# Performance work log

Measured on AMD Instinct MI355X. Metric: run time of the kernel, lower is better.

Reference implementation:

```python
import jax, jax.numpy as jnp
import numpy as np

D_MODEL = 1024
N_HEADS = 16


def setup_inputs() -> dict:
    key = jax.random.key(0)
    ks = jax.random.split(key, 16)
    B, L, S, D = 4, 2048, 2048, D_MODEL
    inp = {
        "q": jax.random.normal(ks[0], (B, L, D), jnp.float32),
        "k": jax.random.normal(ks[1], (B, S, D), jnp.float32),
        "v": jax.random.normal(ks[2], (B, S, D), jnp.float32),
        "tau": jax.random.uniform(ks[3], (B, 1), jnp.float32, 0.5, 1.5),
        "delta": jax.random.normal(ks[4], (B, S), jnp.float32),
    }
    s = 1.0 / np.sqrt(D)
    inp["Wq"] = jax.random.normal(ks[5], (D, D), jnp.float32) * s
    inp["bq"] = jnp.zeros((D,), jnp.float32)
    inp["Wk"] = jax.random.normal(ks[6], (D, D), jnp.float32) * s
    inp["bk"] = jnp.zeros((D,), jnp.float32)
    inp["Wv"] = jax.random.normal(ks[7], (D, D), jnp.float32) * s
    inp["bv"] = jnp.zeros((D,), jnp.float32)
    inp["Wo"] = jax.random.normal(ks[8], (D, D), jnp.float32) * s
    inp["bo"] = jnp.zeros((D,), jnp.float32)
    return inp


def reference(q, k, v, tau, delta, Wq, bq, Wk, bk, Wv, bv, Wo, bo):
    B, L, D = q.shape
    S = k.shape[1]
    H = N_HEADS
    E = D // H
    # Linear projections (torch Linear: x @ W.T + b), split heads
    qh = (q @ Wq.T + bq).reshape(B, L, H, E)
    kh = (k @ Wk.T + bk).reshape(B, S, H, E)
    vh = (v @ Wv.T + bv).reshape(B, S, H, E)
    scale = 1.0 / np.sqrt(E).astype(np.float32)
    # de-stationary attention: scores * tau + delta, then scaled softmax
    scores = jnp.einsum('blhe,bshe->bhls', qh, kh)
    scores = scores * tau[:, None, None, :] + delta[:, None, None, :]
    a = jax.nn.softmax(scale * scores, axis=-1)  # dropout: eval mode (identity)
    out = jnp.einsum('bhls,bshd->blhd', a, vh).reshape(B, L, D)
    return out @ Wo.T + bo
```

## Files before the change

kernel.cpp:

```cpp
#include <hip/hip_runtime.h>
#include <hip/hip_bf16.h>
#include <stdint.h>

typedef unsigned short u16;
typedef __attribute__((ext_vector_type(8))) short short8;
typedef __attribute__((ext_vector_type(4))) short short4v;
typedef __attribute__((ext_vector_type(4))) float f32x4;
typedef __attribute__((ext_vector_type(2))) unsigned int uint2v;

#define DEV static __device__ __forceinline__

DEV u16 f2bf(float f) {
  union { float f; unsigned u; } x; x.f = f;
  unsigned r = x.u + 0x7FFFu + ((x.u >> 16) & 1u);
  return (u16)(r >> 16);
}

DEV unsigned cvtpk_bf16(float a, float b) {
  unsigned r;
  asm("v_cvt_pk_bf16_f32 %0, %1, %2" : "=v"(r) : "v"(a), "v"(b));
  return r;
}

DEV void gld_lds16(const void* g, void* l) {
  __builtin_amdgcn_global_load_lds(
      (const __attribute__((address_space(1))) unsigned int*)(g),
      (__attribute__((address_space(3))) unsigned int*)(l),
      16, 0, 0);
}

__global__ void cvt3(const float* __restrict__ a, const float* __restrict__ b,
                     const float* __restrict__ c, u16* __restrict__ oa,
                     u16* __restrict__ ob, u16* __restrict__ oc, int n4) {
  int i = blockIdx.x * blockDim.x + threadIdx.x;
  if (i >= n4) return;
  const float* in = (blockIdx.y == 0) ? a : (blockIdx.y == 1) ? b : c;
  u16* out = (blockIdx.y == 0) ? oa : (blockIdx.y == 1) ? ob : oc;
  float4 v = ((const float4*)in)[i];
  short4v o;
  o[0] = (short)f2bf(v.x); o[1] = (short)f2bf(v.y);
  o[2] = (short)f2bf(v.z); o[3] = (short)f2bf(v.w);
  ((short4v*)out)[i] = o;
}

__global__ void cvt4(const float* __restrict__ a, const float* __restrict__ b,
                     const float* __restrict__ c, const float* __restrict__ d,
                     u16* __restrict__ oa, u16* __restrict__ ob,
                     u16* __restrict__ oc, u16* __restrict__ od, int n4) {
  int i = blockIdx.x * blockDim.x + threadIdx.x;
  if (i >= n4) return;
  const float* in = (blockIdx.y == 0) ? a : (blockIdx.y == 1) ? b : (blockIdx.y == 2) ? c : d;
  u16* out = (blockIdx.y == 0) ? oa : (blockIdx.y == 1) ? ob : (blockIdx.y == 2) ? oc : od;
  float4 v = ((const float4*)in)[i];
  short4v o;
  o[0] = (short)f2bf(v.x); o[1] = (short)f2bf(v.y);
  o[2] = (short)f2bf(v.z); o[3] = (short)f2bf(v.w);
  ((short4v*)out)[i] = o;
}

__global__ void scale_delta(const float* __restrict__ in, float* __restrict__ out, int n4) {
  int i = blockIdx.x * blockDim.x + threadIdx.x;
  if (i >= n4) return;
  constexpr float C = 0.125f * 1.44269504f;
  float4 v = ((const float4*)in)[i];
  f32x4 o = {v.x * C, v.y * C, v.z * C, v.w * C};
  ((f32x4*)out)[i] = o;
}

template<int OMODE>
__global__ __launch_bounds__(256, 2)
void gemm_nt(const u16* __restrict__ A, const u16* __restrict__ Bt,
             const float* __restrict__ bias, void* __restrict__ out) {
  constexpr int Mn = 8192, Nn = 1024, Kn = 1024;
  constexpr int BM = 128, BN = 128, BK = 64;
  __shared__ __align__(16) u16 As[BM * BK];
  __shared__ __align__(16) u16 Bs[BN * BK];
  constexpr int nbn = Nn / BN;
  constexpr int nwg = (Mn / BM) * nbn;
  int bid = blockIdx.x;
  int swz = (bid & 7) * (nwg >> 3) + (bid >> 3);
  int bm = (swz / nbn) * BM;
  int bn = (swz % nbn) * BN;
  int tid = threadIdx.x;
  int lane = tid & 63, w = tid >> 6;
  int l15 = lane & 15, l4 = lane >> 4;
  int wm = (w >> 1) * 64, wn = (w & 1) * 64;
  int swl = (w << 6);

  f32x4 acc[4][4];
#pragma unroll
  for (int i = 0; i < 4; ++i)
#pragma unroll
    for (int j = 0; j < 4; ++j) acc[i][j] = (f32x4){0.f, 0.f, 0.f, 0.f};

  const u16* Ag = A + (size_t)bm * Kn;
  const u16* Bg = Bt + (size_t)bn * Kn;

  for (int kt = 0; kt < Kn / BK; ++kt) {
    int k0 = kt * BK;
#pragma unroll
    for (int j = 0; j < 4; ++j) {
      int flat = j * 256 + tid;
      int row = flat >> 3, u = flat & 7;
      int gu = u ^ (row & 7);
      gld_lds16(Ag + (size_t)row * Kn + k0 + gu * 8, &As[(j * 256 + swl) * 8]);
    }
#pragma unroll
    for (int j = 0; j < 4; ++j) {
      int flat = j * 256 + tid;
      int row = flat >> 3, u = flat & 7;
      int gu = u ^ (row & 7);
      gld_lds16(Bg + (size_t)row * Kn + k0 + gu * 8, &Bs[(j * 256 + swl) * 8]);
    }
    __syncthreads();
#pragma unroll
    for (int ks = 0; ks < 2; ++ks) {
      short8 af[4], bfr[4];
#pragma unroll
      for (int i = 0; i < 4; ++i) {
        int ra = wm + i * 16 + l15;
        int ua = (ks * 4 + l4) ^ (ra & 7);
        af[i] = *(const short8*)&As[ra * 64 + ua * 8];
        int rb = wn + i * 16 + l15;
        int ub = (ks * 4 + l4) ^ (rb & 7);
        bfr[i] = *(const short8*)&Bs[rb * 64 + ub * 8];
      }
#pragma unroll
      for (int mi = 0; mi < 4; ++mi)
#pragma unroll
        for (int ni = 0; ni < 4; ++ni)
          acc[mi][ni] = __builtin_amdgcn_mfma_f32_16x16x32_bf16(af[mi], bfr[ni], acc[mi][ni], 0, 0, 0);
    }
    __syncthreads();
  }

#pragma unroll
  for (int ni = 0; ni < 4; ++ni) {
    int n = bn + wn + ni * 16 + l15;
    float bv = bias[n];
    int h = n >> 6, e = n & 63;
#pragma unroll
    for (int mi = 0; mi < 4; ++mi) {
      int m0 = bm + wm + mi * 16 + l4 * 4;
      if (OMODE == 2) {
        float* o = (float*)out;
#pragma unroll
        for (int j = 0; j < 4; ++j)
          o[(size_t)(m0 + j) * Nn + n] = acc[mi][ni][j] + bv;
      } else if (OMODE == 0) {
        u16* o = (u16*)out;
#pragma unroll
        for (int j = 0; j < 4; ++j) {
          int m = m0 + j;
          int b = m >> 11, l = m & 2047;
          int idx = ((b * 16 + h) * 2048 + l) * 64 + e;
          o[idx] = f2bf(acc[mi][ni][j] + bv);
        }
      } else {
        u16* o = (u16*)out;
        int b = m0 >> 11, s = m0 & 2047;
        short4v pk;
#pragma unroll
        for (int j = 0; j < 4; ++j) pk[j] = (short)f2bf(acc[mi][ni][j] + bv);
        int idx = ((b * 16 + h) * 64 + e) * 2048 + s;
        *(short4v*)&o[idx] = pk;
      }
    }
  }
}

__global__ __launch_bounds__(512, 6)
void flash_attn(const u16* __restrict__ qh, const u16* __restrict__ kh,
                const u16* __restrict__ vt, const float* __restrict__ tau,
                const float* __restrict__ dl2g, u16* __restrict__ attn) {
  constexpr int S = 2048, E = 64;
  __shared__ __align__(16) u16 Ks[2][64 * 64];
  __shared__ __align__(16) u16 Vs[2][64 * 64];
  __shared__ __align__(16) float dls[2][64];
  __shared__ __align__(16) u16 Ps[8][16 * 72];

  int bh = blockIdx.x & 63, qb = blockIdx.x >> 6;
  int b = bh >> 4, h = bh & 15;
  int tid = threadIdx.x, lane = tid & 63, w = tid >> 6;
  int l15 = lane & 15, l4 = lane >> 4;
  int q0 = qb * 128 + w * 16;

  int srow = tid >> 3, su = tid & 7, sgu = su ^ (srow & 7);
  u16* ldsKbase0 = &Ks[0][(size_t)(w * 64) * 8];
  u16* ldsKbase1 = &Ks[1][(size_t)(w * 64) * 8];
  u16* ldsVbase0 = &Vs[0][(size_t)(w * 64) * 8];
  u16* ldsVbase1 = &Vs[1][(size_t)(w * 64) * 8];

  const u16* Qg = qh + ((size_t)bh * S + q0) * E;
  short8 qf[2];
  qf[0] = *(const short8*)&Qg[l15 * E + l4 * 8];
  qf[1] = *(const short8*)&Qg[l15 * E + 32 + l4 * 8];

  float st2 = tau[b] * (0.125f * 1.44269504f);
  float l_run = 0.f;
  f32x4 oacc[4];
#pragma unroll
  for (int i = 0; i < 4; ++i) oacc[i] = (f32x4){0.f, 0.f, 0.f, 0.f};

  const u16* Kg = kh + (size_t)bh * S * E;
  const u16* Vg = vt + (size_t)bh * E * S;
  const float* Dg = dl2g + (size_t)b * S;

  gld_lds16(Kg + (size_t)srow * E + sgu * 8, ldsKbase0);
  gld_lds16(Vg + (size_t)srow * S + sgu * 8, ldsVbase0);
  if (tid < 16) gld_lds16(Dg + tid * 4, &dls[0][0]);
  __syncthreads();

  for (int t = 0; t < S / 64; ++t) {
    int cur = t & 1;
    if (t < S / 64 - 1) {
      int s1 = (t + 1) * 64;
      gld_lds16(Kg + (size_t)(s1 + srow) * E + sgu * 8, cur ? ldsKbase0 : ldsKbase1);
      gld_lds16(Vg + (size_t)srow * S + s1 + sgu * 8, cur ? ldsVbase0 : ldsVbase1);
      if (tid < 16) gld_lds16(Dg + s1 + tid * 4, &dls[cur ^ 1][0]);
    }

    f32x4 sc[4];
#pragma unroll
    for (int i = 0; i < 4; ++i) sc[i] = (f32x4){0.f, 0.f, 0.f, 0.f};
    __builtin_amdgcn_s_setprio(1);
#pragma unroll
    for (int ks = 0; ks < 2; ++ks) {
#pragma unroll
      for (int sg = 0; sg < 4; ++sg) {
        int sr = sg * 16 + l15;
        int u = (ks * 4 + l4) ^ (sr & 7);
        short8 kf = *(const short8*)&Ks[cur][sr * 64 + u * 8];
        sc[sg] = __builtin_amdgcn_mfma_f32_16x16x32_bf16(kf, qf[ks], sc[sg], 0, 0, 0);
      }
    }
    __builtin_amdgcn_s_setprio(0);

    float psum = 0.f;
#pragma unroll
    for (int sg = 0; sg < 4; ++sg) {
      f32x4 dlv = *(const f32x4*)&dls[cur][sg * 16 + l4 * 4];
      float p0 = __builtin_amdgcn_exp2f(sc[sg][0] * st2 + dlv[0]);
      float p1 = __builtin_amdgcn_exp2f(sc[sg][1] * st2 + dlv[1]);
      float p2 = __builtin_amdgcn_exp2f(sc[sg][2] * st2 + dlv[2]);
      float p3 = __builtin_amdgcn_exp2f(sc[sg][3] * st2 + dlv[3]);
      psum += (p0 + p1) + (p2 + p3);
      uint2v pk;
      pk[0] = cvtpk_bf16(p0, p1);
      pk[1] = cvtpk_bf16(p2, p3);
      *(uint2v*)&Ps[w][l15 * 72 + sg * 16 + l4 * 4] = pk;
    }
    psum += __shfl_xor(psum, 16);
    psum += __shfl_xor(psum, 32);
    l_run += psum;

    __builtin_amdgcn_s_setprio(1);
#pragma unroll
    for (int ks = 0; ks < 2; ++ks) {
      short8 pf = *(const short8*)&Ps[w][l15 * 72 + ks * 32 + l4 * 8];
#pragma unroll
      for (int ni = 0; ni < 4; ++ni) {
        int er = ni * 16 + l15;
        int u = (ks * 4 + l4) ^ (er & 7);
        short8 vf = *(const short8*)&Vs[cur][er * 64 + u * 8];
        oacc[ni] = __builtin_amdgcn_mfma_f32_16x16x32_bf16(pf, vf, oacc[ni], 0, 0, 0);
      }
    }
    __builtin_amdgcn_s_setprio(0);
    __syncthreads();
  }

  float li[4];
#pragma unroll
  for (int j = 0; j < 4; ++j) li[j] = 1.f / __shfl(l_run, l4 * 4 + j);
#pragma unroll
  for (int ni = 0; ni < 4; ++ni) {
    int e = ni * 16 + l15;
#pragma unroll
    for (int j = 0; j < 4; ++j) {
      int l = q0 + l4 * 4 + j;
      size_t idx = (((size_t)b * 2048 + l) * 16 + h) * 64 + e;
      attn[idx] = f2bf(oacc[ni][j] * li[j]);
    }
  }
}

extern "C" void kernel_launch(void* const* d_in, const int* in_sizes, int n_in,
                              void* d_out, int out_size, void* d_ws, size_t ws_size,
                              hipStream_t stream) {
  const float* q = (const float*)d_in[0];
  const float* k = (const float*)d_in[1];
  const float* v = (const float*)d_in[2];
  const float* tau = (const float*)d_in[3];
  const float* delta = (const float*)d_in[4];
  const float* Wq = (const float*)d_in[5];
  const float* bq = (const float*)d_in[6];
  const float* Wk = (const float*)d_in[7];
  const float* bk = (const float*)d_in[8];
  const float* Wv = (const float*)d_in[9];
  const float* bv = (const float*)d_in[10];
  const float* Wo = (const float*)d_in[11];
  const float* bo = (const float*)d_in[12];

  const size_t SZ_ACT = (size_t)8192 * 1024 * 2;
  const size_t SZ_W = (size_t)1024 * 1024 * 2;
  char* p = (char*)d_ws;
  u16* qbf = (u16*)p; p += SZ_ACT;
  u16* kbf = (u16*)p; p += SZ_ACT;
  u16* vbf = (u16*)p; p += SZ_ACT;
  u16* wq = (u16*)p; p += SZ_W;
  u16* wk = (u16*)p; p += SZ_W;
  u16* wv = (u16*)p; p += SZ_W;
  u16* wo = (u16*)p; p += SZ_W;
  float* dl2g = (float*)p; p += 8192 * 4;
  u16* qhb = (u16*)p; p += SZ_ACT;
  u16* khb = (u16*)p; p += SZ_ACT;
  u16* vtb = (u16*)p; p += SZ_ACT;
  u16* attn = qbf;

  cvt3<<<dim3(8192, 3), 256, 0, stream>>>(q, k, v, qbf, kbf, vbf, 2097152);
  cvt4<<<dim3(1024, 4), 256, 0, stream>>>(Wq, Wk, Wv, Wo, wq, wk, wv, wo, 262144);
  scale_delta<<<8, 256, 0, stream>>>(delta, dl2g, 2048);

  gemm_nt<0><<<512, 256, 0, stream>>>(qbf, wq, bq, qhb);
  gemm_nt<0><<<512, 256, 0, stream>>>(kbf, wk, bk, khb);
  gemm_nt<1><<<512, 256, 0, stream>>>(vbf, wv, bv, vtb);
  flash_attn<<<1024, 512, 0, stream>>>(qhb, khb, vtb, tau, dl2g, attn);
  gemm_nt<2><<<512, 256, 0, stream>>>(attn, wo, bo, d_out);
}
```

Measured before the change: 222.5 us.

## Switch flash attention to 32x32x16 MFMA with register-resident P via permlane swap

Rewrites the attention inner loop to use 32x32x16 bf16 MFMAs, with each wave handling 32 query rows instead of 16, which halves the grid to 512 blocks. The probability tile stays in registers: it is repacked with v_permlane32_swap instead of going through an LDS round trip, which removes the per-wave Ps buffer and its LDS traffic. Each K/V tile loaded into LDS now feeds twice as many query rows, and the output store is vectorized. In exchange, register pressure rises, so launch bounds drop to 4 waves per SIMD, and the smaller grid lowers occupancy and parallelism.

```diff
diff --git a/kernel.cpp b/kernel.cpp
--- a/kernel.cpp
+++ b/kernel.cpp
@@ -6,7 +6,9 @@
 typedef __attribute__((ext_vector_type(8))) short short8;
 typedef __attribute__((ext_vector_type(4))) short short4v;
 typedef __attribute__((ext_vector_type(4))) float f32x4;
+typedef __attribute__((ext_vector_type(16))) float f32x16;
 typedef __attribute__((ext_vector_type(2))) unsigned int uint2v;
+typedef __attribute__((ext_vector_type(4))) unsigned int uint4v;
 
 #define DEV static __device__ __forceinline__
 
@@ -20,6 +22,10 @@
   unsigned r;
   asm("v_cvt_pk_bf16_f32 %0, %1, %2" : "=v"(r) : "v"(a), "v"(b));
   return r;
+}
+
+DEV void pl32swap(unsigned& a, unsigned& b) {
+  asm("v_permlane32_swap_b32 %0, %1" : "+v"(a), "+v"(b));
 }
 
 DEV void gld_lds16(const void* g, void* l) {
@@ -27,6 +33,11 @@
       (const __attribute__((address_space(1))) unsigned int*)(g),
       (__attribute__((address_space(3))) unsigned int*)(l),
       16, 0, 0);
+}
+
+DEV f32x16 zero16() {
+  f32x16 z = {0.f,0.f,0.f,0.f,0.f,0.f,0.f,0.f,0.f,0.f,0.f,0.f,0.f,0.f,0.f,0.f};
+  return z;
 }
 
 __global__ void cvt3(const float* __restrict__ a, const float* __restrict__ b,
@@ -169,7 +180,33 @@
   }
 }
 
-__global__ __launch_bounds__(512, 6)
+DEV float softpack(const f32x16 sc, float st2, const float* dlp, int hi,
+                   short8& f0, short8& f1) {
+  float pe[16];
+#pragma unroll
+  for (int g = 0; g < 4; ++g) {
+    f32x4 dlv = *(const f32x4*)(dlp + g * 8 + hi * 4);
+#pragma unroll
+    for (int m = 0; m < 4; ++m)
+      pe[g * 4 + m] = __builtin_amdgcn_exp2f(sc[g * 4 + m] * st2 + dlv[m]);
+  }
+  float ps = 0.f;
+#pragma unroll
+  for (int i = 0; i < 16; i += 4) ps += (pe[i] + pe[i + 1]) + (pe[i + 2] + pe[i + 3]);
+  unsigned a0 = cvtpk_bf16(pe[0], pe[1]), a1 = cvtpk_bf16(pe[2], pe[3]);
+  unsigned b0 = cvtpk_bf16(pe[4], pe[5]), b1 = cvtpk_bf16(pe[6], pe[7]);
+  pl32swap(a0, b0);
+  pl32swap(a1, b1);
+  f0 = __builtin_bit_cast(short8, (uint4v){a0, a1, b0, b1});
+  unsigned c0 = cvtpk_bf16(pe[8], pe[9]), c1 = cvtpk_bf16(pe[10], pe[11]);
+  unsigned d0 = cvtpk_bf16(pe[12], pe[13]), d1 = cvtpk_bf16(pe[14], pe[15]);
+  pl32swap(c0, d0);
+  pl32swap(c1, d1);
+  f1 = __builtin_bit_cast(short8, (uint4v){c0, c1, d0, d1});
+  return ps;
+}
+
+__global__ __launch_bounds__(512, 4)
 void flash_attn(const u16* __restrict__ qh, const u16* __restrict__ kh,
                 const u16* __restrict__ vt, const float* __restrict__ tau,
                 const float* __restrict__ dl2g, u16* __restrict__ attn) {
@@ -177,111 +214,88 @@
   __shared__ __align__(16) u16 Ks[2][64 * 64];
   __shared__ __align__(16) u16 Vs[2][64 * 64];
   __shared__ __align__(16) float dls[2][64];
-  __shared__ __align__(16) u16 Ps[8][16 * 72];
 
   int bh = blockIdx.x & 63, qb = blockIdx.x >> 6;
   int b = bh >> 4, h = bh & 15;
   int tid = threadIdx.x, lane = tid & 63, w = tid >> 6;
-  int l15 = lane & 15, l4 = lane >> 4;
-  int q0 = qb * 128 + w * 16;
-
-  int srow = tid >> 3, su = tid & 7, sgu = su ^ (srow & 7);
-  u16* ldsKbase0 = &Ks[0][(size_t)(w * 64) * 8];
-  u16* ldsKbase1 = &Ks[1][(size_t)(w * 64) * 8];
-  u16* ldsVbase0 = &Vs[0][(size_t)(w * 64) * 8];
-  u16* ldsVbase1 = &Vs[1][(size_t)(w * 64) * 8];
+  int l31 = lane & 31, hi = lane >> 5;
+  int q0 = qb * 256 + w * 32;
+
+  int srow = tid >> 3, sgu = (tid & 7) ^ ((tid >> 3) & 7);
 
   const u16* Qg = qh + ((size_t)bh * S + q0) * E;
-  short8 qf[2];
-  qf[0] = *(const short8*)&Qg[l15 * E + l4 * 8];
-  qf[1] = *(const short8*)&Qg[l15 * E + 32 + l4 * 8];
+  short8 qf[4];
+#pragma unroll
+  for (int ec = 0; ec < 4; ++ec)
+    qf[ec] = *(const short8*)&Qg[l31 * E + ec * 16 + hi * 8];
 
   float st2 = tau[b] * (0.125f * 1.44269504f);
   float l_run = 0.f;
-  f32x4 oacc[4];
-#pragma unroll
-  for (int i = 0; i < 4; ++i) oacc[i] = (f32x4){0.f, 0.f, 0.f, 0.f};
+  f32x16 oa0 = zero16(), oa1 = zero16();
 
   const u16* Kg = kh + (size_t)bh * S * E;
   const u16* Vg = vt + (size_t)bh * E * S;
   const float* Dg = dl2g + (size_t)b * S;
 
-  gld_lds16(Kg + (size_t)srow * E + sgu * 8, ldsKbase0);
-  gld_lds16(Vg + (size_t)srow * S + sgu * 8, ldsVbase0);
+  gld_lds16(Kg + (size_t)srow * E + sgu * 8, &Ks[0][w * 512]);
+  gld_lds16(Vg + (size_t)srow * S + sgu * 8, &Vs[0][w * 512]);
   if (tid < 16) gld_lds16(Dg + tid * 4, &dls[0][0]);
   __syncthreads();
 
   for (int t = 0; t < S / 64; ++t) {
-    int cur = t & 1;
+    int cur = t & 1, nxt = cur ^ 1;
     if (t < S / 64 - 1) {
       int s1 = (t + 1) * 64;
-      gld_lds16(Kg + (size_t)(s1 + srow) * E + sgu * 8, cur ? ldsKbase0 : ldsKbase1);
-      gld_lds16(Vg + (size_t)srow * S + s1 + sgu * 8, cur ? ldsVbase0 : ldsVbase1);
-      if (tid < 16) gld_lds16(Dg + s1 + tid * 4, &dls[cur ^ 1][0]);
-    }
-
-    f32x4 sc[4];
-#pragma unroll
-    for (int i = 0; i < 4; ++i) sc[i] = (f32x4){0.f, 0.f, 0.f, 0.f};
+      gld_lds16(Kg + (size_t)(s1 + srow) * E + sgu * 8, &Ks[nxt][w * 512]);
+      gld_lds16(Vg + (size_t)srow * S + s1 + sgu * 8, &Vs[nxt][w * 512]);
+      if (tid < 16) gld_lds16(Dg + s1 + tid * 4, &dls[nxt][0]);
+    }
+
+    const char* KsB = (const char*)&Ks[cur][0];
+    f32x16 sc0 = zero16(), sc1 = zero16();
     __builtin_amdgcn_s_setprio(1);
 #pragma unroll
-    for (int ks = 0; ks < 2; ++ks) {
-#pragma unroll
-      for (int sg = 0; sg < 4; ++sg) {
-        int sr = sg * 16 + l15;
-        int u = (ks * 4 + l4) ^ (sr & 7);
-        short8 kf = *(const short8*)&Ks[cur][sr * 64 + u * 8];
-        sc[sg] = __builtin_amdgcn_mfma_f32_16x16x32_bf16(kf, qf[ks], sc[sg], 0, 0, 0);
-      }
+    for (int ec = 0; ec < 4; ++ec) {
+      int uo = (((ec * 2 + hi) ^ (l31 & 7)) * 16) + l31 * 128;
+      short8 kf0 = *(const short8*)(KsB + uo);
+      short8 kf1 = *(const short8*)(KsB + 4096 + uo);
+      sc0 = __builtin_amdgcn_mfma_f32_32x32x16_bf16(kf0, qf[ec], sc0, 0, 0, 0);
+      sc1 = __builtin_amdgcn_mfma_f32_32x32x16_bf16(kf1, qf[ec], sc1, 0, 0, 0);
     }
     __builtin_amdgcn_s_setprio(0);
 
-    float psum = 0.f;
-#pragma unroll
-    for (int sg = 0; sg < 4; ++sg) {
-      f32x4 dlv = *(const f32x4*)&dls[cur][sg * 16 + l4 * 4];
-      float p0 = __builtin_amdgcn_exp2f(sc[sg][0] * st2 + dlv[0]);
-      float p1 = __builtin_amdgcn_exp2f(sc[sg][1] * st2 + dlv[1]);
-      float p2 = __builtin_amdgcn_exp2f(sc[sg][2] * st2 + dlv[2]);
-      float p3 = __builtin_amdgcn_exp2f(sc[sg][3] * st2 + dlv[3]);
-      psum += (p0 + p1) + (p2 + p3);
-      uint2v pk;
-      pk[0] = cvtpk_bf16(p0, p1);
-      pk[1] = cvtpk_bf16(p2, p3);
-      *(uint2v*)&Ps[w][l15 * 72 + sg * 16 + l4 * 4] = pk;
-    }
-    psum += __shfl_xor(psum, 16);
+    short8 pf0, pf1, pf2, pf3;
+    float psum = softpack(sc0, st2, &dls[cur][0], hi, pf0, pf1);
+    psum += softpack(sc1, st2, &dls[cur][32], hi, pf2, pf3);
     psum += __shfl_xor(psum, 32);
     l_run += psum;
 
+    const char* VsB = (const char*)&Vs[cur][0];
     __builtin_amdgcn_s_setprio(1);
 #pragma unroll
-    for (int ks = 0; ks < 2; ++ks) {
-      short8 pf = *(const short8*)&Ps[w][l15 * 72 + ks * 32 + l4 * 8];
-#pragma unroll
-      for (int ni = 0; ni < 4; ++ni) {
-        int er = ni * 16 + l15;
-        int u = (ks * 4 + l4) ^ (er & 7);
-        short8 vf = *(const short8*)&Vs[cur][er * 64 + u * 8];
-        oacc[ni] = __builtin_amdgcn_mfma_f32_16x16x32_bf16(pf, vf, oacc[ni], 0, 0, 0);
-      }
+    for (int ksb = 0; ksb < 4; ++ksb) {
+      int uo = (((ksb * 2 + hi) ^ (l31 & 7)) * 16) + l31 * 128;
+      short8 v0 = *(const short8*)(VsB + uo);
+      short8 v1 = *(const short8*)(VsB + 4096 + uo);
+      short8 pf = (ksb == 0) ? pf0 : (ksb == 1) ? pf1 : (ksb == 2) ? pf2 : pf3;
+      oa0 = __builtin_amdgcn_mfma_f32_32x32x16_bf16(v0, pf, oa0, 0, 0, 0);
+      oa1 = __builtin_amdgcn_mfma_f32_32x32x16_bf16(v1, pf, oa1, 0, 0, 0);
     }
     __builtin_amdgcn_s_setprio(0);
     __syncthreads();
   }
 
-  float li[4];
-#pragma unroll
-  for (int j = 0; j < 4; ++j) li[j] = 1.f / __shfl(l_run, l4 * 4 + j);
-#pragma unroll
-  for (int ni = 0; ni < 4; ++ni) {
-    int e = ni * 16 + l15;
-#pragma unroll
-    for (int j = 0; j < 4; ++j) {
-      int l = q0 + l4 * 4 + j;
-      size_t idx = (((size_t)b * 2048 + l) * 16 + h) * 64 + e;
-      attn[idx] = f2bf(oacc[ni][j] * li[j]);
-    }
+  float li = 1.f / l_run;
+  u16* Og = attn + ((((size_t)b * 2048 + q0 + l31) * 16 + h) * 64);
+#pragma unroll
+  for (int g = 0; g < 4; ++g) {
+    uint2v s0, s1;
+    s0[0] = cvtpk_bf16(oa0[g * 4 + 0] * li, oa0[g * 4 + 1] * li);
+    s0[1] = cvtpk_bf16(oa0[g * 4 + 2] * li, oa0[g * 4 + 3] * li);
+    *(uint2v*)&Og[g * 8 + hi * 4] = s0;
+    s1[0] = cvtpk_bf16(oa1[g * 4 + 0] * li, oa1[g * 4 + 1] * li);
+    s1[1] = cvtpk_bf16(oa1[g * 4 + 2] * li, oa1[g * 4 + 3] * li);
+    *(uint2v*)&Og[32 + g * 8 + hi * 4] = s1;
   }
 }
 
@@ -325,6 +339,6 @@
   gemm_nt<0><<<512, 256, 0, stream>>>(qbf, wq, bq, qhb);
   gemm_nt<0><<<512, 256, 0, stream>>>(kbf, wk, bk, khb);
   gemm_nt<1><<<512, 256, 0, stream>>>(vbf, wv, bv, vtb);
-  flash_attn<<<1024, 512, 0, stream>>>(qhb, khb, vtb, tau, dl2g, attn);
+  flash_attn<<<512, 512, 0, stream>>>(qhb, khb, vtb, tau, dl2g, attn);
   gemm_nt<2><<<512, 256, 0, stream>>>(attn, wo, bo, d_out);
 }
```

After: 213.1 us. 4.2% less time.
